# Kernel tuning notes

Measured on AMD Instinct MI355X. Metric: run time of the kernel, lower is better.

## Reference

```python
import math
import jax, jax.numpy as jnp
import numpy as np

B, S, HID = 1, 2048, 2048
H, D = 32, 64            # heads, head_dim = HID // H
THETA = 10000.0
EPS = 1e-6
LAYER_IDX = 12
LAM_INIT = 0.8 - 0.6 * math.exp(-0.3 * LAYER_IDX)  # lambda_init_fn(layer_idx)
SCALE = 1.0 / math.sqrt(D)


def _rope_cos_sin(seq_len, dim):
    inv_freq = 1.0 / (THETA ** (np.arange(0, dim, 2, dtype=np.float64) / dim))
    freqs = np.outer(np.arange(seq_len, dtype=np.float64), inv_freq)
    emb = np.concatenate([freqs, freqs], axis=-1)  # [S, D] (llama duplicates freqs)
    return jnp.asarray(np.cos(emb), jnp.float32), jnp.asarray(np.sin(emb), jnp.float32)


def _rotate_half(x):
    return jnp.concatenate([-x[..., D // 2:], x[..., : D // 2]], axis=-1)


def _apply_rope(x, cos, sin):
    # x: [B, H, S, D]; cos/sin: [S, D] broadcast over B, H
    return x * cos + _rotate_half(x) * sin


def setup_inputs() -> dict:
    key = jax.random.key(0)
    ks = jax.random.split(key, 10)
    return {
        "hidden_states": jax.random.normal(ks[0], (B, S, HID), jnp.float32),
        "Wq": jax.random.normal(ks[1], (2 * HID, HID), jnp.float32) * 0.02,
        "Wk": jax.random.normal(ks[2], (2 * HID, HID), jnp.float32) * 0.02,
        "Wv": jax.random.normal(ks[3], (HID, HID), jnp.float32) * 0.02,
        "Wo": jax.random.normal(ks[4], (HID, HID), jnp.float32) * 0.02,
        "lambda_q1": jax.random.normal(ks[5], (D,), jnp.float32) * 0.1,
        "lambda_k1": jax.random.normal(ks[6], (D,), jnp.float32) * 0.1,
        "lambda_q2": jax.random.normal(ks[7], (D,), jnp.float32) * 0.1,
        "lambda_k2": jax.random.normal(ks[8], (D,), jnp.float32) * 0.1,
        "subln_w": jnp.ones((D,), jnp.float32),
    }


def reference(hidden_states, Wq, Wk, Wv, Wo,
              lambda_q1, lambda_k1, lambda_q2, lambda_k2, subln_w):
    # Projections (nn.Linear, no bias): x @ W.T
    q = hidden_states @ Wq.T                       # [B, S, 2*HID]
    k = hidden_states @ Wk.T                       # [B, S, 2*HID]
    v = hidden_states @ Wv.T                       # [B, S, HID]

    def to_heads(t):  # [B, S, H*D] -> [B, H, S, D]
        return t.reshape(B, S, H, D).transpose(0, 2, 1, 3)

    q1, q2 = jnp.split(q, 2, axis=-1)
    k1, k2 = jnp.split(k, 2, axis=-1)
    q1, q2, k1, k2, v = map(to_heads, (q1, q2, k1, k2, v))

    cos, sin = _rope_cos_sin(S, D)
    q1, k1 = _apply_rope(q1, cos, sin), _apply_rope(k1, cos, sin)
    q2, k2 = _apply_rope(q2, cos, sin), _apply_rope(k2, cos, sin)

    # Causal additive mask [S, S]
    causal = jnp.tril(jnp.ones((S, S), bool))
    neg_inf = jnp.finfo(jnp.float32).min
    mask = jnp.where(causal, 0.0, neg_inf)

    s1 = jnp.einsum("bhqd,bhkd->bhqk", q1, k1) * SCALE + mask
    s2 = jnp.einsum("bhqd,bhkd->bhqk", q2, k2) * SCALE + mask

    lam = (jnp.exp(jnp.sum(lambda_q1 * lambda_k1))
           - jnp.exp(jnp.sum(lambda_q2 * lambda_k2)) + LAM_INIT)

    attn_w = jax.nn.softmax(s1, axis=-1) - lam * jax.nn.softmax(s2, axis=-1)
    attn = jnp.einsum("bhqk,bhkd->bhqd", attn_w, v)  # [B, H, S, D]

    # Head-wise RMSNorm (LlamaRMSNorm over value_head_dim)
    var = jnp.mean(jnp.square(attn), axis=-1, keepdims=True)
    attn = attn * jax.lax.rsqrt(var + EPS) * subln_w
    attn = attn * (1.0 - LAM_INIT)

    out = attn.transpose(0, 2, 1, 3).reshape(B, S, HID) @ Wo.T
    return out
```

## Files before the change

kernel.cpp:

```cpp
#include <hip/hip_runtime.h>


typedef __bf16 bf16;
typedef __bf16 bf16x4 __attribute__((ext_vector_type(4)));
typedef __bf16 bf16x8 __attribute__((ext_vector_type(8)));
typedef float  f32x4  __attribute__((ext_vector_type(4)));

#define MFMA(a, b, c) __builtin_amdgcn_mfma_f32_16x16x32_bf16((a), (b), (c), 0, 0, 0)

#define S_LEN   2048
#define HID_DIM 2048
#define NHEAD   32
#define HD      64
#define QKV_N   10240
#define LAM_INIT 0.7836057665316245f
#define ONE_MINUS_LAM_INIT 0.21639423346837553f
#define QSCALE  0.18033688011112042f
#define RMS_EPS 1e-6f

__device__ __forceinline__ void gld16(const void* g, void* l) {
    __builtin_amdgcn_global_load_lds(
        (const __attribute__((address_space(1))) void*)g,
        (__attribute__((address_space(3))) void*)l, 16, 0, 0);
}

__global__ void cvt_all(const float* __restrict__ hs, const float* __restrict__ Wq,
                        const float* __restrict__ Wk, const float* __restrict__ Wv,
                        const float* __restrict__ Wo,
                        const float* __restrict__ lq1, const float* __restrict__ lk1,
                        const float* __restrict__ lq2, const float* __restrict__ lk2,
                        bf16* __restrict__ hsb, bf16* __restrict__ Wb,
                        bf16* __restrict__ Wob, float* __restrict__ lam_out) {
    const int bid = blockIdx.x;
    if (bid >= 28672) {
        const int t = threadIdx.x;
        if (t < 64) {
            float a = lq1[t] * lk1[t];
            float b = lq2[t] * lk2[t];
            #pragma unroll
            for (int off = 32; off > 0; off >>= 1) {
                a += __shfl_xor(a, off, 64);
                b += __shfl_xor(b, off, 64);
            }
            if (t == 0) lam_out[0] = expf(a) - expf(b) + LAM_INIT;
        }
        return;
    }
    const float* src; bf16* dst; int off;
    if      (bid <  4096) { src = hs; dst = hsb;            off = bid;         }
    else if (bid < 12288) { src = Wq; dst = Wb;             off = bid - 4096;  }
    else if (bid < 20480) { src = Wk; dst = Wb +  8388608;  off = bid - 12288; }
    else if (bid < 24576) { src = Wv; dst = Wb + 16777216;  off = bid - 20480; }
    else                  { src = Wo; dst = Wob;            off = bid - 24576; }
    const int i = off * 1024 + threadIdx.x * 4;
    float4 v = *(const float4*)(src + i);
    bf16x4 o = { (bf16)v.x, (bf16)v.y, (bf16)v.z, (bf16)v.w };
    *(bf16x4*)(dst + i) = o;
}

template<int OUT_MODE>
__global__ __launch_bounds__(256, 3)
void gemm_bt(const bf16* __restrict__ A, const bf16* __restrict__ B,
             void* __restrict__ Cout, int M, int N, int K_total, int K_part) {
    __shared__ __align__(16) bf16 As[128 * 64];
    __shared__ __align__(16) bf16 Bs[128 * 64];
    const int tid  = threadIdx.x;
    const int wave = tid >> 6, lane = tid & 63;
    const int wm = wave >> 1, wn = wave & 1;
    const int l = lane & 15, quad = lane >> 4;
    const int m0 = blockIdx.y * 128, n0 = blockIdx.x * 128;
    const int kz = blockIdx.z * K_part;

    f32x4 acc[4][4];
    #pragma unroll
    for (int i = 0; i < 4; ++i)
        #pragma unroll
        for (int j = 0; j < 4; ++j) acc[i][j] = (f32x4){0.f, 0.f, 0.f, 0.f};

    const int rr  = tid >> 3;
    const int csw = ((tid & 7) ^ (rr & 7)) * 8;
    const bf16* Ag = A + (size_t)(m0 + rr) * K_total + kz + csw;
    const bf16* Bg = B + (size_t)(n0 + rr) * K_total + kz + csw;

    for (int kt = 0; kt < K_part; kt += 64) {
        __syncthreads();
        #pragma unroll
        for (int j = 0; j < 4; ++j) {
            gld16(Ag + (size_t)(32 * j) * K_total + kt, As + j * 2048 + tid * 8);
            gld16(Bg + (size_t)(32 * j) * K_total + kt, Bs + j * 2048 + tid * 8);
        }
        __syncthreads();

        #pragma unroll
        for (int ks = 0; ks < 2; ++ks) {
            const int co = (((ks << 2) | quad) ^ (l & 7)) << 3;
            bf16x8 af[4], bfr[4];
            #pragma unroll
            for (int mi = 0; mi < 4; ++mi)
                af[mi] = *(const bf16x8*)(As + (wm * 64 + mi * 16 + l) * 64 + co);
            #pragma unroll
            for (int ni = 0; ni < 4; ++ni)
                bfr[ni] = *(const bf16x8*)(Bs + (wn * 64 + ni * 16 + l) * 64 + co);
            #pragma unroll
            for (int mi = 0; mi < 4; ++mi)
                #pragma unroll
                for (int ni = 0; ni < 4; ++ni)
                    acc[mi][ni] = MFMA(af[mi], bfr[ni], acc[mi][ni]);
        }
    }

    float* Pf = (OUT_MODE == 2)
              ? ((float*)Cout + (size_t)blockIdx.z * M * N) : (float*)Cout;
    #pragma unroll
    for (int mi = 0; mi < 4; ++mi)
        #pragma unroll
        for (int ni = 0; ni < 4; ++ni)
            #pragma unroll
            for (int r = 0; r < 4; ++r) {
                const int row = m0 + wm * 64 + mi * 16 + quad * 4 + r;
                const int col = n0 + wn * 64 + ni * 16 + l;
                const float v = acc[mi][ni][r];
                if (OUT_MODE == 1) ((bf16*)Cout)[(size_t)row * N + col] = (bf16)v;
                else               Pf[(size_t)row * N + col] = v;
            }
}

__global__ void reduce_add(const float* __restrict__ p, float* __restrict__ out, int n) {
    const int i = (blockIdx.x * 256 + threadIdx.x) * 4;
    float4 a = *(const float4*)(p + i);
    float4 b = *(const float4*)(p + n + i);
    float4 o = { a.x + b.x, a.y + b.y, a.z + b.z, a.w + b.w };
    *(float4*)(out + i) = o;
}

__global__ __launch_bounds__(256)
void rope_split(const bf16* __restrict__ qkv,
                bf16* __restrict__ Q1, bf16* __restrict__ K1,
                bf16* __restrict__ Q2, bf16* __restrict__ K2,
                bf16* __restrict__ Vt) {
    const int h = blockIdx.y;
    const int s0 = blockIdx.x * 64;
    const int t = threadIdx.x;
    const int d = t & 63, sr = t >> 6;
    __shared__ __align__(16) bf16 vt_lds[64][72];

    const int i = d & 31;
    const float invf = exp2f(-(float)i * 0.4152410118609203f);
    const float sign = (d < 32) ? -1.0f : 1.0f;

    for (int it = 0; it < 16; ++it) {
        const int s = s0 + it * 4 + sr;
        const bf16* row = qkv + (size_t)s * QKV_N;
        const int cb  = h * 64 + d;
        const int cbo = h * 64 + (d ^ 32);
        const float ang = (float)s * invf;
        const float cs = cosf(ang), sn = sinf(ang);
        const float q1v = (float)row[cb],         q1o = (float)row[cbo];
        const float q2v = (float)row[2048 + cb],  q2o = (float)row[2048 + cbo];
        const float k1v = (float)row[4096 + cb],  k1o = (float)row[4096 + cbo];
        const float k2v = (float)row[6144 + cb],  k2o = (float)row[6144 + cbo];
        const float vv  = (float)row[8192 + cb];
        const size_t o = ((size_t)h * S_LEN + s) * HD + d;
        Q1[o] = (bf16)((q1v * cs + sign * q1o * sn) * QSCALE);
        Q2[o] = (bf16)((q2v * cs + sign * q2o * sn) * QSCALE);
        K1[o] = (bf16)(k1v * cs + sign * k1o * sn);
        K2[o] = (bf16)(k2v * cs + sign * k2o * sn);
        vt_lds[d][it * 4 + sr] = (bf16)vv;
    }
    __syncthreads();
    const int dd = t >> 2, cg = t & 3;
    bf16x8 w0 = *(const bf16x8*)(&vt_lds[dd][cg * 16]);
    bf16x8 w1 = *(const bf16x8*)(&vt_lds[dd][cg * 16 + 8]);
    bf16* dst = Vt + ((size_t)h * HD + dd) * S_LEN + s0 + cg * 16;
    *(bf16x8*)(dst)     = w0;
    *(bf16x8*)(dst + 8) = w1;
}

__global__ __launch_bounds__(256, 2)
void diff_attn(const bf16* __restrict__ Q1, const bf16* __restrict__ K1,
               const bf16* __restrict__ Q2, const bf16* __restrict__ K2,
               const bf16* __restrict__ Vt, const float* __restrict__ lam_p,
               const float* __restrict__ subln_w, bf16* __restrict__ attn_out) {
    const int bid  = blockIdx.x;
    const int h    = (bid >> 1) & 31;
    const int idx  = bid >> 6;
    const int qb   = (bid & 1) ? idx : (15 - idx);
    const int q0   = qb * 128;
    const int tid  = threadIdx.x;
    const int wave = tid >> 6, lane = tid & 63;
    const int sid  = wave >> 1, half = wave & 1;
    const int l    = lane & 15, quad = lane >> 4;
    const int q0w  = q0 + half * 64;

    __shared__ __align__(16) char smem[61440];
    bf16* K1s = (bf16*)smem;
    bf16* K2s = (bf16*)(smem + 8192);
    bf16* Vts = (bf16*)(smem + 16384);
    bf16* Pw  = (bf16*)(smem + 24576 + wave * 9216);

    const bf16* Qh  = (sid ? Q2 : Q1) + ((size_t)h * S_LEN + q0w) * HD;
    const bf16* K1g = K1 + (size_t)h * S_LEN * HD;
    const bf16* K2g = K2 + (size_t)h * S_LEN * HD;
    const bf16* Vtg = Vt + (size_t)h * HD * S_LEN;
    const bf16* Ksm = sid ? K2s : K1s;

    const int rr  = tid >> 3;
    const int csw = ((tid & 7) ^ (rr & 7)) * 8;
    bf16* l1 = K1s + tid * 8;
    bf16* l2 = K2s + tid * 8;
    bf16* lv = Vts + tid * 8;

    bf16x8 qf[4][2];
    #pragma unroll
    for (int ni = 0; ni < 4; ++ni)
        #pragma unroll
        for (int ks = 0; ks < 2; ++ks)
            qf[ni][ks] = *(const bf16x8*)(Qh + (ni * 16 + l) * HD + ks * 32 + quad * 8);

    f32x4 O[4][4];
    #pragma unroll
    for (int mi = 0; mi < 4; ++mi)
        #pragma unroll
        for (int ni = 0; ni < 4; ++ni)
            O[mi][ni] = (f32x4){0.f, 0.f, 0.f, 0.f};
    float csum[4] = {0.f, 0.f, 0.f, 0.f};

    const int T = 2 * qb + 2;
    const int sw8 = l & 7;
    for (int t = 0; t < T; ++t) {
        const int kv0 = t * 64;
        __syncthreads();
        {
            const bf16* k1p = K1g + (size_t)(kv0 + rr) * HD + csw;
            const bf16* k2p = K2g + (size_t)(kv0 + rr) * HD + csw;
            const bf16* vtp = Vtg + (size_t)rr * S_LEN + kv0 + csw;
            gld16(k1p, l1);
            gld16(k1p + (size_t)32 * HD, l1 + 2048);
            gld16(k2p, l2);
            gld16(k2p + (size_t)32 * HD, l2 + 2048);
            gld16(vtp, lv);
            gld16(vtp + (size_t)32 * S_LEN, lv + 2048);
        }
        __syncthreads();

        if (kv0 <= q0w) {
            const bool diag = (kv0 == q0w);

            #pragma unroll
            for (int mi = 0; mi < 4; ++mi) {
                const int krow = (mi * 16 + l) * 64;
                bf16x8 ka0 = *(const bf16x8*)(Ksm + krow + ((quad ^ sw8) << 3));
                bf16x8 ka1 = *(const bf16x8*)(Ksm + krow + (((4 + quad) ^ sw8) << 3));
                #pragma unroll
                for (int ni = 0; ni < 4; ++ni) {
                    f32x4 c = (f32x4){0.f, 0.f, 0.f, 0.f};
                    c = MFMA(ka0, qf[ni][0], c);
                    c = MFMA(ka1, qf[ni][1], c);
                    bf16x4 pk;
                    float lsum = 0.f;
                    #pragma unroll
                    for (int r = 0; r < 4; ++r) {
                        float p = __builtin_amdgcn_exp2f(c[r]);
                        if (diag && (mi * 16 + quad * 4 + r > ni * 16 + l)) p = 0.f;
                        lsum += p;
                        pk[r] = (bf16)p;
                    }
                    csum[ni] += lsum;
                    *(bf16x4*)(Pw + (ni * 16 + l) * 72 + mi * 16 + quad * 4) = pk;
                }
            }

            bf16x8 vb[2][4];
            #pragma unroll
            for (int ks = 0; ks < 2; ++ks)
                #pragma unroll
                for (int ni = 0; ni < 4; ++ni)
                    vb[ks][ni] = *(const bf16x8*)(Vts + (ni * 16 + l) * 64 +
                                                  ((((ks << 2) + quad) ^ sw8) << 3));

            asm volatile("s_waitcnt lgkmcnt(0)" ::: "memory");

            #pragma unroll
            for (int ks = 0; ks < 2; ++ks) {
                bf16x8 pa[4];
                #pragma unroll
                for (int mi = 0; mi < 4; ++mi)
                    pa[mi] = *(const bf16x8*)(Pw + (mi * 16 + l) * 72 + ks * 32 + quad * 8);
                #pragma unroll
                for (int ni = 0; ni < 4; ++ni)
                    #pragma unroll
                    for (int mi = 0; mi < 4; ++mi)
                        O[mi][ni] = MFMA(pa[mi], vb[ks][ni], O[mi][ni]);
            }
        }
    }

    __syncthreads();
    float* epi = (float*)(smem + half * 16640);

    #pragma unroll
    for (int ni = 0; ni < 4; ++ni) {
        csum[ni] += __shfl_xor(csum[ni], 16, 64);
        csum[ni] += __shfl_xor(csum[ni], 32, 64);
    }

    if (sid == 1) {
        const float lam = lam_p[0];
        #pragma unroll
        for (int mi = 0; mi < 4; ++mi)
            #pragma unroll
            for (int r = 0; r < 4; ++r) {
                const float inv = lam / __shfl(csum[mi], quad * 4 + r, 64);
                const int row = mi * 16 + quad * 4 + r;
                #pragma unroll
                for (int ni = 0; ni < 4; ++ni)
                    epi[row * 65 + ni * 16 + l] = O[mi][ni][r] * inv;
            }
    }
    __syncthreads();

    if (sid == 0) {
        float sw[4];
        #pragma unroll
        for (int ni = 0; ni < 4; ++ni) sw[ni] = subln_w[ni * 16 + l];

        #pragma unroll
        for (int mi = 0; mi < 4; ++mi) {
            float inv1[4];
            #pragma unroll
            for (int r = 0; r < 4; ++r)
                inv1[r] = 1.0f / __shfl(csum[mi], quad * 4 + r, 64);

            float v[4][4]; float ssq[4] = {0.f, 0.f, 0.f, 0.f};
            #pragma unroll
            for (int ni = 0; ni < 4; ++ni)
                #pragma unroll
                for (int r = 0; r < 4; ++r) {
                    const int row = mi * 16 + quad * 4 + r;
                    const float x = O[mi][ni][r] * inv1[r] - epi[row * 65 + ni * 16 + l];
                    v[ni][r] = x;
                    ssq[r] += x * x;
                }
            #pragma unroll
            for (int r = 0; r < 4; ++r) {
                float s = ssq[r];
                s += __shfl_xor(s, 1, 64);
                s += __shfl_xor(s, 2, 64);
                s += __shfl_xor(s, 4, 64);
                s += __shfl_xor(s, 8, 64);
                ssq[r] = rsqrtf(s * (1.0f / 64.0f) + RMS_EPS) * ONE_MINUS_LAM_INIT;
            }
            #pragma unroll
            for (int ni = 0; ni < 4; ++ni)
                #pragma unroll
                for (int r = 0; r < 4; ++r) {
                    const int row = q0w + mi * 16 + quad * 4 + r;
                    attn_out[(size_t)row * HID_DIM + h * 64 + ni * 16 + l] =
                        (bf16)(v[ni][r] * ssq[r] * sw[ni]);
                }
        }
    }
}

extern "C" void kernel_launch(void* const* d_in, const int* in_sizes, int n_in,
                              void* d_out, int out_size, void* d_ws, size_t ws_size,
                              hipStream_t stream) {
    const float* hs  = (const float*)d_in[0];
    const float* Wq  = (const float*)d_in[1];
    const float* Wk  = (const float*)d_in[2];
    const float* Wv  = (const float*)d_in[3];
    const float* Wo  = (const float*)d_in[4];
    const float* lq1 = (const float*)d_in[5];
    const float* lk1 = (const float*)d_in[6];
    const float* lq2 = (const float*)d_in[7];
    const float* lk2 = (const float*)d_in[8];
    const float* slw = (const float*)d_in[9];

    if (ws_size < 151000000u) return;

    char* ws = (char*)d_ws;
    bf16*  hsb  = (bf16*)(ws);
    bf16*  Wb   = (bf16*)(ws + 8388608);
    bf16*  Wob  = (bf16*)(ws + 50331648);
    bf16*  qkv  = (bf16*)(ws + 58720256);
    float* part = (float*)(ws + 58720256);
    bf16*  Q1b  = (bf16*)(ws + 100663296);
    bf16*  K1b  = (bf16*)(ws + 109051904);
    bf16*  Q2b  = (bf16*)(ws + 117440512);
    bf16*  K2b  = (bf16*)(ws + 125829120);
    bf16*  Vtb  = (bf16*)(ws + 134217728);
    bf16*  abuf = (bf16*)(ws + 142606336);
    float* lamp = (float*)(ws + 150994944);

    cvt_all<<<28673, 256, 0, stream>>>(hs, Wq, Wk, Wv, Wo, lq1, lk1, lq2, lk2,
                                       hsb, Wb, Wob, lamp);

    gemm_bt<1><<<dim3(QKV_N / 128, S_LEN / 128, 1), 256, 0, stream>>>(
        hsb, Wb, qkv, S_LEN, QKV_N, HID_DIM, HID_DIM);

    rope_split<<<dim3(S_LEN / 64, NHEAD), 256, 0, stream>>>(qkv, Q1b, K1b, Q2b, K2b, Vtb);

    diff_attn<<<512, 256, 0, stream>>>(Q1b, K1b, Q2b, K2b, Vtb, lamp, slw, abuf);

    gemm_bt<2><<<dim3(HID_DIM / 128, S_LEN / 128, 2), 256, 0, stream>>>(
        abuf, Wob, part, S_LEN, HID_DIM, HID_DIM, HID_DIM / 2);
    reduce_add<<<4096, 256, 0, stream>>>(part, (float*)d_out, S_LEN * HID_DIM);
}
```

Baseline: 369.4 us.

## Fuse RoPE, head split and V transpose into QKV GEMM epilogue

The QKV projection GEMM now computes the transposed product (W rows as M side) so each lane holds head-dim columns, and applies RoPE, the Q scale and head split directly in the epilogue. V is written transposed straight from registers. This removes the separate rope_split kernel and the round trip of the 2048x10240 bf16 qkv intermediate through memory. The cost is extra sin/cos work and uncoalesced scalar stores for the Vt transpose inside the GEMM epilogue, plus the use of fast __sinf/__cosf approximations.

```diff
diff --git a/kernel.cpp b/kernel.cpp
--- a/kernel.cpp
+++ b/kernel.cpp
@@ -17,6 +17,7 @@
 #define ONE_MINUS_LAM_INIT 0.21639423346837553f
 #define QSCALE  0.18033688011112042f
 #define RMS_EPS 1e-6f
+#define L2T     0.4152410118609203f
 
 __device__ __forceinline__ void gld16(const void* g, void* l) {
     __builtin_amdgcn_global_load_lds(
@@ -58,10 +59,116 @@
     *(bf16x4*)(dst + i) = o;
 }
 
-template<int OUT_MODE>
 __global__ __launch_bounds__(256, 3)
-void gemm_bt(const bf16* __restrict__ A, const bf16* __restrict__ B,
-             void* __restrict__ Cout, int M, int N, int K_total, int K_part) {
+void qkv_rope_gemm(const bf16* __restrict__ A, const bf16* __restrict__ B,
+                   bf16* __restrict__ Q1, bf16* __restrict__ Q2,
+                   bf16* __restrict__ K1, bf16* __restrict__ K2,
+                   bf16* __restrict__ Vt) {
+    __shared__ __align__(16) bf16 As[128 * 64];
+    __shared__ __align__(16) bf16 Bs[128 * 64];
+    const int tid  = threadIdx.x;
+    const int wave = tid >> 6, lane = tid & 63;
+    const int wm = wave >> 1, wn = wave & 1;
+    const int l = lane & 15, quad = lane >> 4;
+    const int m0 = blockIdx.y * 128, n0 = blockIdx.x * 128;
+
+    f32x4 acc[4][4];
+    #pragma unroll
+    for (int i = 0; i < 4; ++i)
+        #pragma unroll
+        for (int j = 0; j < 4; ++j) acc[i][j] = (f32x4){0.f, 0.f, 0.f, 0.f};
+
+    const int rr  = tid >> 3;
+    const int csw = ((tid & 7) ^ (rr & 7)) * 8;
+    const bf16* Ag = A + (size_t)(m0 + rr) * HID_DIM + csw;
+    const bf16* Bg = B + (size_t)(n0 + rr) * HID_DIM + csw;
+
+    for (int kt = 0; kt < HID_DIM; kt += 64) {
+        __syncthreads();
+        #pragma unroll
+        for (int j = 0; j < 4; ++j) {
+            gld16(Ag + (size_t)(32 * j) * HID_DIM + kt, As + j * 2048 + tid * 8);
+            gld16(Bg + (size_t)(32 * j) * HID_DIM + kt, Bs + j * 2048 + tid * 8);
+        }
+        __syncthreads();
+
+        #pragma unroll
+        for (int ks = 0; ks < 2; ++ks) {
+            const int co = (((ks << 2) | quad) ^ (l & 7)) << 3;
+            bf16x8 hf[4], wf[4];
+            #pragma unroll
+            for (int hi = 0; hi < 4; ++hi)
+                hf[hi] = *(const bf16x8*)(As + (wm * 64 + hi * 16 + l) * 64 + co);
+            #pragma unroll
+            for (int wi = 0; wi < 4; ++wi)
+                wf[wi] = *(const bf16x8*)(Bs + (wn * 64 + wi * 16 + l) * 64 + co);
+            #pragma unroll
+            for (int wi = 0; wi < 4; ++wi)
+                #pragma unroll
+                for (int hi = 0; hi < 4; ++hi)
+                    acc[wi][hi] = MFMA(wf[wi], hf[hi], acc[wi][hi]);
+        }
+    }
+
+    const int c = n0 + wn * 64;
+    const int sbase = m0 + wm * 64;
+    bf16* dst; int off; float scale = 1.0f; bool isv = false;
+    if      (c < 2048) { dst = Q1; off = c;        scale = QSCALE; }
+    else if (c < 4096) { dst = Q2; off = c - 2048; scale = QSCALE; }
+    else if (c < 6144) { dst = K1; off = c - 4096; }
+    else if (c < 8192) { dst = K2; off = c - 6144; }
+    else               { isv = true; off = c - 8192; }
+    const int h = off >> 6;
+
+    if (!isv) {
+        float invf[2][4];
+        #pragma unroll
+        for (int p = 0; p < 2; ++p)
+            #pragma unroll
+            for (int r = 0; r < 4; ++r)
+                invf[p][r] = exp2f(-(float)(p * 16 + quad * 4 + r) * L2T);
+
+        #pragma unroll
+        for (int hi = 0; hi < 4; ++hi) {
+            const float s = (float)(sbase + hi * 16 + l);
+            float cs[2][4], sn[2][4];
+            #pragma unroll
+            for (int p = 0; p < 2; ++p)
+                #pragma unroll
+                for (int r = 0; r < 4; ++r) {
+                    const float ang = s * invf[p][r];
+                    cs[p][r] = __cosf(ang);
+                    sn[p][r] = __sinf(ang);
+                }
+            bf16* rowp = dst + ((size_t)h * S_LEN + sbase + hi * 16 + l) * HD + quad * 4;
+            #pragma unroll
+            for (int wi = 0; wi < 4; ++wi) {
+                const int p = wi & 1;
+                const float sign = (wi < 2) ? -1.0f : 1.0f;
+                bf16x4 o;
+                #pragma unroll
+                for (int r = 0; r < 4; ++r)
+                    o[r] = (bf16)((acc[wi][hi][r] * cs[p][r] +
+                                   sign * acc[wi ^ 2][hi][r] * sn[p][r]) * scale);
+                *(bf16x4*)(rowp + wi * 16) = o;
+            }
+        }
+    } else {
+        #pragma unroll
+        for (int wi = 0; wi < 4; ++wi)
+            #pragma unroll
+            for (int r = 0; r < 4; ++r) {
+                bf16* vrow = Vt + ((size_t)h * HD + wi * 16 + quad * 4 + r) * S_LEN + sbase;
+                #pragma unroll
+                for (int hi = 0; hi < 4; ++hi)
+                    vrow[hi * 16 + l] = (bf16)acc[wi][hi][r];
+            }
+    }
+}
+
+__global__ __launch_bounds__(256, 3)
+void gemm_bt_splitk(const bf16* __restrict__ A, const bf16* __restrict__ B,
+                    float* __restrict__ Cout, int M, int N, int K_total, int K_part) {
     __shared__ __align__(16) bf16 As[128 * 64];
     __shared__ __align__(16) bf16 Bs[128 * 64];
     const int tid  = threadIdx.x;
@@ -109,8 +216,7 @@
         }
     }
 
-    float* Pf = (OUT_MODE == 2)
-              ? ((float*)Cout + (size_t)blockIdx.z * M * N) : (float*)Cout;
+    float* Pf = Cout + (size_t)blockIdx.z * M * N;
     #pragma unroll
     for (int mi = 0; mi < 4; ++mi)
         #pragma unroll
@@ -119,9 +225,7 @@
             for (int r = 0; r < 4; ++r) {
                 const int row = m0 + wm * 64 + mi * 16 + quad * 4 + r;
                 const int col = n0 + wn * 64 + ni * 16 + l;
-                const float v = acc[mi][ni][r];
-                if (OUT_MODE == 1) ((bf16*)Cout)[(size_t)row * N + col] = (bf16)v;
-                else               Pf[(size_t)row * N + col] = v;
+                Pf[(size_t)row * N + col] = acc[mi][ni][r];
             }
 }
 
@@ -131,49 +235,6 @@
     float4 b = *(const float4*)(p + n + i);
     float4 o = { a.x + b.x, a.y + b.y, a.z + b.z, a.w + b.w };
     *(float4*)(out + i) = o;
-}
-
-__global__ __launch_bounds__(256)
-void rope_split(const bf16* __restrict__ qkv,
-                bf16* __restrict__ Q1, bf16* __restrict__ K1,
-                bf16* __restrict__ Q2, bf16* __restrict__ K2,
-                bf16* __restrict__ Vt) {
-    const int h = blockIdx.y;
-    const int s0 = blockIdx.x * 64;
-    const int t = threadIdx.x;
-    const int d = t & 63, sr = t >> 6;
-    __shared__ __align__(16) bf16 vt_lds[64][72];
-
-    const int i = d & 31;
-    const float invf = exp2f(-(float)i * 0.4152410118609203f);
-    const float sign = (d < 32) ? -1.0f : 1.0f;
-
-    for (int it = 0; it < 16; ++it) {
-        const int s = s0 + it * 4 + sr;
-        const bf16* row = qkv + (size_t)s * QKV_N;
-        const int cb  = h * 64 + d;
-        const int cbo = h * 64 + (d ^ 32);
-        const float ang = (float)s * invf;
-        const float cs = cosf(ang), sn = sinf(ang);
-        const float q1v = (float)row[cb],         q1o = (float)row[cbo];
-        const float q2v = (float)row[2048 + cb],  q2o = (float)row[2048 + cbo];
-        const float k1v = (float)row[4096 + cb],  k1o = (float)row[4096 + cbo];
-        const float k2v = (float)row[6144 + cb],  k2o = (float)row[6144 + cbo];
-        const float vv  = (float)row[8192 + cb];
-        const size_t o = ((size_t)h * S_LEN + s) * HD + d;
-        Q1[o] = (bf16)((q1v * cs + sign * q1o * sn) * QSCALE);
-        Q2[o] = (bf16)((q2v * cs + sign * q2o * sn) * QSCALE);
-        K1[o] = (bf16)(k1v * cs + sign * k1o * sn);
-        K2[o] = (bf16)(k2v * cs + sign * k2o * sn);
-        vt_lds[d][it * 4 + sr] = (bf16)vv;
-    }
-    __syncthreads();
-    const int dd = t >> 2, cg = t & 3;
-    bf16x8 w0 = *(const bf16x8*)(&vt_lds[dd][cg * 16]);
-    bf16x8 w1 = *(const bf16x8*)(&vt_lds[dd][cg * 16 + 8]);
-    bf16* dst = Vt + ((size_t)h * HD + dd) * S_LEN + s0 + cg * 16;
-    *(bf16x8*)(dst)     = w0;
-    *(bf16x8*)(dst + 8) = w1;
 }
 
 __global__ __launch_bounds__(256, 2)
@@ -382,7 +443,6 @@
     bf16*  hsb  = (bf16*)(ws);
     bf16*  Wb   = (bf16*)(ws + 8388608);
     bf16*  Wob  = (bf16*)(ws + 50331648);
-    bf16*  qkv  = (bf16*)(ws + 58720256);
     float* part = (float*)(ws + 58720256);
     bf16*  Q1b  = (bf16*)(ws + 100663296);
     bf16*  K1b  = (bf16*)(ws + 109051904);
@@ -395,14 +455,12 @@
     cvt_all<<<28673, 256, 0, stream>>>(hs, Wq, Wk, Wv, Wo, lq1, lk1, lq2, lk2,
                                        hsb, Wb, Wob, lamp);
 
-    gemm_bt<1><<<dim3(QKV_N / 128, S_LEN / 128, 1), 256, 0, stream>>>(
-        hsb, Wb, qkv, S_LEN, QKV_N, HID_DIM, HID_DIM);
-
-    rope_split<<<dim3(S_LEN / 64, NHEAD), 256, 0, stream>>>(qkv, Q1b, K1b, Q2b, K2b, Vtb);
+    qkv_rope_gemm<<<dim3(QKV_N / 128, S_LEN / 128), 256, 0, stream>>>(
+        hsb, Wb, Q1b, Q2b, K1b, K2b, Vtb);
 
     diff_attn<<<512, 256, 0, stream>>>(Q1b, K1b, Q2b, K2b, Vtb, lamp, slw, abuf);
 
-    gemm_bt<2><<<dim3(HID_DIM / 128, S_LEN / 128, 2), 256, 0, stream>>>(
+    gemm_bt_splitk<<<dim3(HID_DIM / 128, S_LEN / 128, 2), 256, 0, stream>>>(
         abuf, Wob, part, S_LEN, HID_DIM, HID_DIM, HID_DIM / 2);
     reduce_add<<<4096, 256, 0, stream>>>(part, (float*)d_out, S_LEN * HID_DIM);
 }
```

After: 361.6 us. 2.1% less time.
